# Kernel optimization log

Measured on AMD Instinct MI355X. Metric: run time of the kernel, lower is better.

## Reference

```python
import jax, jax.numpy as jnp
import numpy as np


def _mlp(x, w1, b1, w2, b2):
    # x: [..., in]; torch Linear: y = x @ W.T + b; GELU is exact (erf) in torch default
    h = jax.nn.gelu(x @ w1.T + b1, approximate=False)
    return h @ w2.T + b2


def setup_inputs() -> dict:
    key = jax.random.key(0)
    ks = jax.random.split(key, 12)
    b, dim, e, h, w = 8, 64, 128, 256, 256
    nt, nb = 6, 8
    inp = {
        "x": jax.random.normal(ks[0], (b, dim, h, w), jnp.float32),
        "flux": jax.random.normal(ks[1], (b, e, h, w), jnp.float32),
        "prompt": jax.random.uniform(ks[2], (nt, nb, e), jnp.float32),
        "conv_w": jax.random.normal(ks[3], (e, e, 3, 3), jnp.float32) * 0.02,
        "b_fc1_w": jax.random.normal(ks[4], (nb, dim), jnp.float32) * 0.05,
        "b_fc1_b": jax.random.normal(ks[5], (nb,), jnp.float32) * 0.05,
        "b_fc2_w": jax.random.normal(ks[6], (nb, nb), jnp.float32) * 0.05,
        "b_fc2_b": jax.random.normal(ks[7], (nb,), jnp.float32) * 0.05,
        "t_fc1_w": jax.random.normal(ks[8], (nt, e), jnp.float32) * 0.05,
        "t_fc1_b": jax.random.normal(ks[9], (nt,), jnp.float32) * 0.05,
        "t_fc2_w": jax.random.normal(ks[10], (nt, nt), jnp.float32) * 0.05,
        "t_fc2_b": jax.random.normal(ks[11], (nt,), jnp.float32) * 0.05,
    }
    return inp


def reference(x, flux, prompt, conv_w, b_fc1_w, b_fc1_b, b_fc2_w, b_fc2_b,
              t_fc1_w, t_fc1_b, t_fc2_w, t_fc2_b):
    # x: [b, dim, h, w]; flux: [b, embed_dim, h, w]
    flux = jnp.where(jnp.isnan(flux), jnp.zeros_like(flux), flux)
    x_hw = jnp.transpose(x, (0, 2, 3, 1))       # [b,h,w,dim]
    flux_hw = jnp.transpose(flux, (0, 2, 3, 1))  # [b,h,w,e]

    # per-pixel routing weights (softmax over basis / task channels)
    x_basis = jax.nn.softmax(_mlp(x_hw, b_fc1_w, b_fc1_b, b_fc2_w, b_fc2_b), axis=-1)   # [b,h,w,nb]
    x_task = jax.nn.softmax(_mlp(flux_hw, t_fc1_w, t_fc1_b, t_fc2_w, t_fc2_b), axis=-1)  # [b,h,w,nt]

    # fused two-stage broadcast-multiply-reduce:
    # sum_t sum_k x_task[b,t,h,w] * x_basis[b,k,h,w] * prompt[t,k,e] -> [b,e,h,w]
    prompts = jnp.einsum('bhwt,bhwk,tke->behw', x_task, x_basis, prompt)

    # conv3x3, stride 1, padding 1, no bias (NCHW, OIHW)
    out = jax.lax.conv_general_dilated(
        prompts, conv_w, window_strides=(1, 1), padding=((1, 1), (1, 1)),
        dimension_numbers=('NCHW', 'OIHW', 'NCHW'))
    return out
```

## Files before the change

### kernel.cpp

```cpp
#include <hip/hip_runtime.h>
#include <hip/hip_bf16.h>
#include <math.h>

#define HW   65536
#define NPIX 524288
#define NB   8
#define NT   6
#define NC   48
#define DIM  64
#define EE   128
#define KSTEPS 14
#define KVALID 432
#define COLS 130

typedef short bf16x8 __attribute__((ext_vector_type(8)));
typedef float f32x4  __attribute__((ext_vector_type(4)));

__device__ __forceinline__ float gelu_exact(float v) {
    return 0.5f * v * (1.0f + erff(v * 0.70710678118654752f));
}

__device__ __forceinline__ unsigned pack_bf16(float v0, float v1) {
    __hip_bfloat16 h0 = __float2bfloat16(v0);
    __hip_bfloat16 h1 = __float2bfloat16(v1);
    return (unsigned)(*(unsigned short*)&h0) | ((unsigned)(*(unsigned short*)&h1) << 16);
}

__global__ __launch_bounds__(256) void fold_weights_kernel(
    const float* __restrict__ conv_w,
    const float* __restrict__ prompt,
    unsigned short* __restrict__ WfB)
{
    int f = blockIdx.x * 256 + threadIdx.x;
    int j    = f & 7;
    int lane = (f >> 3) & 63;
    int ob   = (f >> 9) & 7;
    int ks   = f >> 12;

    int o = ob * 16 + (lane & 15);
    int k = ks * 32 + ((lane >> 4) << 3) + j;

    float acc = 0.f;
    if (k < KVALID) {
        int tap = k / 48;
        int tk  = k - tap * 48;
        int dy = tap / 3;
        int dx = tap - dy * 3;
        const float* pw = conv_w + ((size_t)o * EE) * 9 + dy * 3 + dx;
        const float* pp = prompt + (size_t)tk * EE;
        #pragma unroll 4
        for (int e = 0; e < EE; ++e)
            acc += pw[(size_t)e * 9] * pp[e];
    }
    __hip_bfloat16 h = __float2bfloat16(acc);
    WfB[f] = *(unsigned short*)&h;
}

__global__ __launch_bounds__(256) void routing_kernel(
    const float* __restrict__ x,
    const float* __restrict__ flux,
    const float* __restrict__ b1w, const float* __restrict__ b1b,
    const float* __restrict__ b2w, const float* __restrict__ b2b,
    const float* __restrict__ t1w, const float* __restrict__ t1b,
    const float* __restrict__ t2w, const float* __restrict__ t2b,
    uint4* __restrict__ c2)
{
    __shared__ float s_b1w[DIM * 8];
    __shared__ float s_t1w[EE * 8];
    __shared__ float s_b2w[64];
    __shared__ float s_t2w[36];
    __shared__ float s_b1b[8], s_b2b[8], s_t1b[8], s_t2b[8];

    int tid = threadIdx.x;
    for (int i = tid; i < DIM * 8; i += 256) {
        int ci = i >> 3, j = i & 7;
        s_b1w[i] = b1w[j * DIM + ci];
    }
    for (int i = tid; i < EE * 8; i += 256) {
        int ci = i >> 3, j = i & 7;
        s_t1w[i] = (j < NT) ? t1w[j * EE + ci] : 0.f;
    }
    if (tid < 64) s_b2w[tid] = b2w[tid];
    if (tid < 36) s_t2w[tid] = t2w[tid];
    if (tid < 8) {
        s_b1b[tid] = b1b[tid];
        s_b2b[tid] = b2b[tid];
        s_t1b[tid] = (tid < NT) ? t1b[tid] : 0.f;
        s_t2b[tid] = (tid < NT) ? t2b[tid] : 0.f;
    }
    __syncthreads();

    int gid = blockIdx.x * 256 + tid;
    int b   = gid >> 16;
    int yx  = gid & (HW - 1);

    const float* fp = flux + (size_t)b * EE * HW + yx;
    const float* xp = x + (size_t)b * DIM * HW + yx;

    float t[6];
    #pragma unroll
    for (int j = 0; j < NT; ++j) t[j] = s_t1b[j];
    #pragma unroll 1
    for (int cb = 0; cb < EE; cb += 8) {
        float v[8];
        #pragma unroll
        for (int u = 0; u < 8; ++u)
            v[u] = fp[(size_t)(cb + u) * HW];
        #pragma unroll
        for (int u = 0; u < 8; ++u) {
            float vv = v[u];
            vv = (vv == vv) ? vv : 0.f;
            float4 wA = *(const float4*)&s_t1w[(cb + u) * 8];
            float2 wB = *(const float2*)&s_t1w[(cb + u) * 8 + 4];
            t[0] += vv * wA.x;
            t[1] += vv * wA.y;
            t[2] += vv * wA.z;
            t[3] += vv * wA.w;
            t[4] += vv * wB.x;
            t[5] += vv * wB.y;
        }
    }

    float a[8];
    #pragma unroll
    for (int j = 0; j < 8; ++j) a[j] = s_b1b[j];
    #pragma unroll 1
    for (int cb = 0; cb < DIM; cb += 8) {
        float v[8];
        #pragma unroll
        for (int u = 0; u < 8; ++u)
            v[u] = xp[(size_t)(cb + u) * HW];
        #pragma unroll
        for (int u = 0; u < 8; ++u) {
            float vv = v[u];
            float4 wa = *(const float4*)&s_b1w[(cb + u) * 8];
            float4 wb = *(const float4*)&s_b1w[(cb + u) * 8 + 4];
            a[0] += vv * wa.x;
            a[1] += vv * wa.y;
            a[2] += vv * wa.z;
            a[3] += vv * wa.w;
            a[4] += vv * wb.x;
            a[5] += vv * wb.y;
            a[6] += vv * wb.z;
            a[7] += vv * wb.w;
        }
    }

    float task[6];
    {
        float gt[6];
        #pragma unroll
        for (int j = 0; j < NT; ++j) gt[j] = gelu_exact(t[j]);
        float tv[6];
        #pragma unroll
        for (int i = 0; i < NT; ++i) {
            float s = s_t2b[i];
            #pragma unroll
            for (int j = 0; j < NT; ++j) s += gt[j] * s_t2w[i * 6 + j];
            tv[i] = s;
        }
        float m = tv[0];
        #pragma unroll
        for (int i = 1; i < NT; ++i) m = fmaxf(m, tv[i]);
        float s = 0.f;
        #pragma unroll
        for (int i = 0; i < NT; ++i) { tv[i] = expf(tv[i] - m); s += tv[i]; }
        float inv = 1.f / s;
        #pragma unroll
        for (int i = 0; i < NT; ++i) task[i] = tv[i] * inv;
    }

    float basis[8];
    {
        float g[8];
        #pragma unroll
        for (int j = 0; j < 8; ++j) g[j] = gelu_exact(a[j]);
        float bv[8];
        #pragma unroll
        for (int i = 0; i < 8; ++i) {
            float s = s_b2b[i];
            #pragma unroll
            for (int j = 0; j < 8; ++j) s += g[j] * s_b2w[i * 8 + j];
            bv[i] = s;
        }
        float m = bv[0];
        #pragma unroll
        for (int i = 1; i < 8; ++i) m = fmaxf(m, bv[i]);
        float s = 0.f;
        #pragma unroll
        for (int i = 0; i < 8; ++i) { bv[i] = expf(bv[i] - m); s += bv[i]; }
        float inv = 1.f / s;
        #pragma unroll
        for (int i = 0; i < 8; ++i) basis[i] = bv[i] * inv;
    }

    #pragma unroll
    for (int j = 0; j < 6; ++j) {
        uint4 q;
        q.x = pack_bf16(task[j] * basis[0], task[j] * basis[1]);
        q.y = pack_bf16(task[j] * basis[2], task[j] * basis[3]);
        q.z = pack_bf16(task[j] * basis[4], task[j] * basis[5]);
        q.w = pack_bf16(task[j] * basis[6], task[j] * basis[7]);
        c2[(size_t)j * NPIX + gid] = q;
    }
}

__global__ __launch_bounds__(256, 3) void conv_kernel(
    const uint4* __restrict__ c2,
    const unsigned short* __restrict__ WfB,
    float* __restrict__ out)
{
    __shared__ uint4 tile4[3120];

    int bid = blockIdx.x;
    int s = bid & 1;
    int y = (bid >> 1) & 255;
    int b = bid >> 9;
    int x0 = s << 7;
    int tid = threadIdx.x;

    #pragma unroll 4
    for (int i = tid; i < 3120; i += 256)
        tile4[i] = make_uint4(0u, 0u, 0u, 0u);
    __syncthreads();

    for (int idx = tid; idx < 2340; idx += 256) {
        int dyc = idx / 130;
        int col = idx - dyc * 130;
        int dy  = dyc / 6;
        int ch  = dyc - dy * 6;
        int gy = y + dy - 1;
        int gx = x0 - 1 + col;
        if ((unsigned)gy < 256u && (unsigned)gx < 256u) {
            uint4 v = c2[(size_t)ch * NPIX + (((size_t)b << 16) + (gy << 8) + gx)];
            int lb = ((dy * COLS + col) << 7) + (ch << 4);
            lb ^= (col & 7) << 4;
            tile4[lb >> 4] = v;
        }
    }
    __syncthreads();

    int lane = tid & 63;
    int wv = tid >> 6;
    int wm = wv & 1;
    int wn = wv >> 1;
    int o0 = wm << 6;
    int nbase = wn << 2;
    int lrow = lane & 15;
    int lk   = lane >> 4;

    f32x4 acc[4][4];
    #pragma unroll
    for (int mi = 0; mi < 4; ++mi)
        #pragma unroll
        for (int ni = 0; ni < 4; ++ni)
            acc[mi][ni] = (f32x4){0.f, 0.f, 0.f, 0.f};

    const char* tbase = (const char*)tile4;

    #pragma unroll
    for (int ks = 0; ks < KSTEPS; ++ks) {
        bf16x8 a[4];
        #pragma unroll
        for (int mi = 0; mi < 4; ++mi)
            a[mi] = *(const bf16x8*)(WfB + ((size_t)((ks * 8) + wm * 4 + mi) * 64 + lane) * 8);

        int k0 = ks * 32 + (lk << 3);
        int tap = k0 / 48;
        if (tap > 8) tap = 8;
        int ch = k0 - tap * 48;
        int dy = tap / 3;
        int dx = tap - dy * 3;

        #pragma unroll
        for (int ni = 0; ni < 4; ++ni) {
            int col = ((nbase + ni) << 4) + lrow + dx;
            int lb = ((dy * COLS + col) << 7) + (ch << 1);
            lb ^= (col & 7) << 4;
            bf16x8 bfr = *(const bf16x8*)(tbase + lb);
            #pragma unroll
            for (int mi = 0; mi < 4; ++mi)
                acc[mi][ni] = __builtin_amdgcn_mfma_f32_16x16x32_bf16(a[mi], bfr, acc[mi][ni], 0, 0, 0);
        }
    }

    int orow = lk << 2;
    #pragma unroll
    for (int mi = 0; mi < 4; ++mi) {
        #pragma unroll
        for (int ni = 0; ni < 4; ++ni) {
            int o = o0 + mi * 16 + orow;
            int xx = x0 + ((nbase + ni) << 4) + lrow;
            float* op = out + (((size_t)(b * 128 + o)) << 16) + (y << 8) + xx;
            #pragma unroll
            for (int r = 0; r < 4; ++r)
                op[(size_t)r << 16] = acc[mi][ni][r];
        }
    }
}

extern "C" void kernel_launch(void* const* d_in, const int* in_sizes, int n_in,
                              void* d_out, int out_size, void* d_ws, size_t ws_size,
                              hipStream_t stream) {
    const float* x      = (const float*)d_in[0];
    const float* flux   = (const float*)d_in[1];
    const float* prompt = (const float*)d_in[2];
    const float* conv_w = (const float*)d_in[3];
    const float* b1w    = (const float*)d_in[4];
    const float* b1b    = (const float*)d_in[5];
    const float* b2w    = (const float*)d_in[6];
    const float* b2b    = (const float*)d_in[7];
    const float* t1w    = (const float*)d_in[8];
    const float* t1b    = (const float*)d_in[9];
    const float* t2w    = (const float*)d_in[10];
    const float* t2b    = (const float*)d_in[11];
    float* out = (float*)d_out;

    char* ws = (char*)d_ws;
    uint4* c2 = (uint4*)ws;
    unsigned short* WfB = (unsigned short*)(ws + (size_t)6 * NPIX * 16);

    fold_weights_kernel<<<224, 256, 0, stream>>>(conv_w, prompt, WfB);
    routing_kernel<<<2048, 256, 0, stream>>>(x, flux, b1w, b1b, b2w, b2b,
                                             t1w, t1b, t2w, t2b, c2);
    conv_kernel<<<4096, 256, 0, stream>>>(c2, WfB, out);
}
```

Before: 234.5 us.

## Stage flux/x channel reads through double-buffered LDS slabs with float4 loads

The routing kernel now loads 16-channel slabs of flux and x into a double-buffered shared-memory tile. Each thread issues float4 global loads while the previous slab is consumed from LDS, so the next slab's fetch overlaps the current slab's FMAs. This replaces per-thread scalar strided loads that were issued 8 channels at a time. It adds a block-wide barrier per slab, 32 KB of LDS per block that may cut occupancy, and moves the bias additions to after accumulation.

```diff
diff --git a/kernel.cpp b/kernel.cpp
--- a/kernel.cpp
+++ b/kernel.cpp
@@ -65,6 +65,7 @@
     const float* __restrict__ t2w, const float* __restrict__ t2b,
     uint4* __restrict__ c2)
 {
+    __shared__ float slab[2][16][256];
     __shared__ float s_b1w[DIM * 8];
     __shared__ float s_t1w[EE * 8];
     __shared__ float s_b2w[64];
@@ -88,63 +89,106 @@
         s_t1b[tid] = (tid < NT) ? t1b[tid] : 0.f;
         s_t2b[tid] = (tid < NT) ? t2b[tid] : 0.f;
     }
+
+    int b   = blockIdx.x >> 8;
+    int px0 = (blockIdx.x & 255) << 8;
+    int gid = blockIdx.x * 256 + tid;
+
+    const float* fbase = flux + (size_t)b * EE * HW + px0;
+    const float* xbase = x    + (size_t)b * DIM * HW + px0;
+
+    int wv4  = (tid >> 6) << 2;
+    int loff = (tid & 63) << 2;
+
+    float t[6], a[8];
+    #pragma unroll
+    for (int j = 0; j < NT; ++j) t[j] = 0.f;
+    #pragma unroll
+    for (int j = 0; j < 8; ++j) a[j] = 0.f;
+
+    float4 st[4];
+
+    {
+        const float* sb = fbase;
+        #pragma unroll
+        for (int i = 0; i < 4; ++i)
+            st[i] = *(const float4*)(sb + (size_t)(wv4 + i) * HW + loff);
+        #pragma unroll
+        for (int i = 0; i < 4; ++i)
+            *(float4*)&slab[0][wv4 + i][loff] = st[i];
+    }
     __syncthreads();
 
-    int gid = blockIdx.x * 256 + tid;
-    int b   = gid >> 16;
-    int yx  = gid & (HW - 1);
-
-    const float* fp = flux + (size_t)b * EE * HW + yx;
-    const float* xp = x + (size_t)b * DIM * HW + yx;
-
-    float t[6];
-    #pragma unroll
-    for (int j = 0; j < NT; ++j) t[j] = s_t1b[j];
     #pragma unroll 1
-    for (int cb = 0; cb < EE; cb += 8) {
-        float v[8];
-        #pragma unroll
-        for (int u = 0; u < 8; ++u)
-            v[u] = fp[(size_t)(cb + u) * HW];
-        #pragma unroll
-        for (int u = 0; u < 8; ++u) {
-            float vv = v[u];
-            vv = (vv == vv) ? vv : 0.f;
-            float4 wA = *(const float4*)&s_t1w[(cb + u) * 8];
-            float2 wB = *(const float2*)&s_t1w[(cb + u) * 8 + 4];
-            t[0] += vv * wA.x;
-            t[1] += vv * wA.y;
-            t[2] += vv * wA.z;
-            t[3] += vv * wA.w;
-            t[4] += vv * wB.x;
-            t[5] += vv * wB.y;
-        }
-    }
-
-    float a[8];
-    #pragma unroll
-    for (int j = 0; j < 8; ++j) a[j] = s_b1b[j];
+    for (int s = 0; s < 8; ++s) {
+        int s1 = s + 1;
+        const float* sb = (s1 < 8) ? (fbase + ((size_t)s1 << 4) * HW)
+                                   : (xbase);
+        #pragma unroll
+        for (int i = 0; i < 4; ++i)
+            st[i] = *(const float4*)(sb + (size_t)(wv4 + i) * HW + loff);
+
+        int pb = s & 1;
+        #pragma unroll
+        for (int c = 0; c < 16; ++c) {
+            float v = slab[pb][c][tid];
+            v = (v == v) ? v : 0.f;
+            const float* wp = &s_t1w[(s * 16 + c) * 8];
+            float4 wA = *(const float4*)wp;
+            float2 wB = *(const float2*)(wp + 4);
+            t[0] += v * wA.x;
+            t[1] += v * wA.y;
+            t[2] += v * wA.z;
+            t[3] += v * wA.w;
+            t[4] += v * wB.x;
+            t[5] += v * wB.y;
+        }
+
+        #pragma unroll
+        for (int i = 0; i < 4; ++i)
+            *(float4*)&slab[pb ^ 1][wv4 + i][loff] = st[i];
+        __syncthreads();
+    }
+
     #pragma unroll 1
-    for (int cb = 0; cb < DIM; cb += 8) {
-        float v[8];
-        #pragma unroll
-        for (int u = 0; u < 8; ++u)
-            v[u] = xp[(size_t)(cb + u) * HW];
-        #pragma unroll
-        for (int u = 0; u < 8; ++u) {
-            float vv = v[u];
-            float4 wa = *(const float4*)&s_b1w[(cb + u) * 8];
-            float4 wb = *(const float4*)&s_b1w[(cb + u) * 8 + 4];
-            a[0] += vv * wa.x;
-            a[1] += vv * wa.y;
-            a[2] += vv * wa.z;
-            a[3] += vv * wa.w;
-            a[4] += vv * wb.x;
-            a[5] += vv * wb.y;
-            a[6] += vv * wb.z;
-            a[7] += vv * wb.w;
-        }
-    }
+    for (int s = 8; s < 12; ++s) {
+        if (s < 11) {
+            const float* sb = xbase + ((size_t)(s - 7) << 4) * HW;
+            #pragma unroll
+            for (int i = 0; i < 4; ++i)
+                st[i] = *(const float4*)(sb + (size_t)(wv4 + i) * HW + loff);
+        }
+
+        int pb = s & 1;
+        int c0 = (s - 8) * 16;
+        #pragma unroll
+        for (int c = 0; c < 16; ++c) {
+            float v = slab[pb][c][tid];
+            const float* wp = &s_b1w[(c0 + c) * 8];
+            float4 wa = *(const float4*)wp;
+            float4 wb = *(const float4*)(wp + 4);
+            a[0] += v * wa.x;
+            a[1] += v * wa.y;
+            a[2] += v * wa.z;
+            a[3] += v * wa.w;
+            a[4] += v * wb.x;
+            a[5] += v * wb.y;
+            a[6] += v * wb.z;
+            a[7] += v * wb.w;
+        }
+
+        if (s < 11) {
+            #pragma unroll
+            for (int i = 0; i < 4; ++i)
+                *(float4*)&slab[pb ^ 1][wv4 + i][loff] = st[i];
+            __syncthreads();
+        }
+    }
+
+    #pragma unroll
+    for (int j = 0; j < NT; ++j) t[j] += s_t1b[j];
+    #pragma unroll
+    for (int j = 0; j < 8; ++j) a[j] += s_b1b[j];
 
     float task[6];
     {
```

New measurement: 255.4 us. 1.09x slower.
